# Performance work log

Hardware: AMD Instinct MI355X
Metric: run time of the kernel (lower is better)

The kernel has to match this reference:

```python
import jax, jax.numpy as jnp
import numpy as np


def setup_inputs() -> dict:
    key = jax.random.key(0)
    ks = jax.random.split(key, 8)
    b, l, d, n = 2, 4096, 1024, 16
    s = 0.02
    return {
        "x": jax.random.normal(ks[0], (b, l, d), dtype=jnp.float32),
        "W1": jax.random.normal(ks[1], (d, d), dtype=jnp.float32) * s,
        "b1": jnp.zeros((d,), dtype=jnp.float32),
        "W2": jax.random.normal(ks[2], (n, d), dtype=jnp.float32) * s,
        "b2": jnp.zeros((n,), dtype=jnp.float32),
        "W3": jax.random.normal(ks[3], (n, d), dtype=jnp.float32) * s,
        "b3": jnp.zeros((n,), dtype=jnp.float32),
        "A": jax.random.normal(ks[4], (d, n), dtype=jnp.float32) * s,
    }


def reference(x, W1, b1, W2, b2, W3, b3, A):
    # Faithful to the torch S6.forward as written:
    #   B = fc2(x); C = fc3(x); delta = softplus(fc1(x))
    #   dB = einsum('bld,bln->bldn', delta, B)
    #   h  = dA * 0 + x[..., None] * dB          (h starts at zeros, no scan)
    #   y  = einsum('bln,bldn->bld', C, h)
    # which collapses exactly to y = x * delta * sum_n(C * B).
    # dA = exp(einsum('bld,dn->bldn', delta, A)) is multiplied by zeros and
    # therefore never influences the output (A is a dead parameter here).
    B = jnp.einsum('bld,nd->bln', x, W2) + b2          # (b, l, n)
    C = jnp.einsum('bld,nd->bln', x, W3) + b3          # (b, l, n)
    delta = jax.nn.softplus(jnp.einsum('bld,ed->ble', x, W1) + b1)  # (b, l, d)
    cb = jnp.sum(C * B, axis=-1)                        # (b, l) = sum_n C*B
    y = x * delta * cb[..., None]                       # (b, l, d)
    return y
```

## Files before the change

### kernel.cpp

```cpp
#include <hip/hip_runtime.h>
#include <hip/hip_bf16.h>
#include <stdint.h>

typedef __attribute__((ext_vector_type(8))) short short8;
typedef __attribute__((ext_vector_type(4))) float f32x4;
typedef __attribute__((ext_vector_type(4))) unsigned short us4;

static __device__ __forceinline__ unsigned short f2bf(float f) {
    union { float f; uint32_t u; } v; v.f = f;
    uint32_t u = v.u;
    uint32_t r = u + 0x7FFFu + ((u >> 16) & 1u);
    return (unsigned short)(r >> 16);
}
static __device__ __forceinline__ float bf2f(unsigned short h) {
    union { uint32_t u; float f; } v; v.u = ((uint32_t)h) << 16;
    return v.f;
}

static __device__ __forceinline__ short8 cvt8(float4 a, float4 b) {
    short8 r;
    r[0] = (short)f2bf(a.x); r[1] = (short)f2bf(a.y);
    r[2] = (short)f2bf(a.z); r[3] = (short)f2bf(a.w);
    r[4] = (short)f2bf(b.x); r[5] = (short)f2bf(b.y);
    r[6] = (short)f2bf(b.z); r[7] = (short)f2bf(b.w);
    return r;
}

__global__ __launch_bounds__(256) void convert_w(const float* __restrict__ w1,
                                                 const float* __restrict__ w2,
                                                 const float* __restrict__ w3,
                                                 unsigned short* __restrict__ o1,
                                                 unsigned short* __restrict__ o2,
                                                 unsigned short* __restrict__ o3) {
    int b = blockIdx.x;
    const float* src; unsigned short* dst; int idx;
    if (b < 1024)      { src = w1; dst = o1; idx = b * 256 + threadIdx.x; }
    else if (b < 1040) { src = w2; dst = o2; idx = (b - 1024) * 256 + threadIdx.x; }
    else               { src = w3; dst = o3; idx = (b - 1040) * 256 + threadIdx.x; }
    float4 v = ((const float4*)src)[idx];
    us4 r = { f2bf(v.x), f2bf(v.y), f2bf(v.z), f2bf(v.w) };
    *(us4*)&dst[(size_t)idx * 4] = r;
}

__global__ __launch_bounds__(256) void cb_kernel(
    const float* __restrict__ x,
    const unsigned short* __restrict__ w2b,
    const unsigned short* __restrict__ w3b,
    const float* __restrict__ b2,
    const float* __restrict__ b3,
    unsigned short* __restrict__ xb,
    float* __restrict__ cbo)
{
    __shared__ float red[4][2][16][16];

    const int t = threadIdx.x;
    const int wave = t >> 6, lane = t & 63;
    const int r0 = blockIdx.x * 16;
    const int rrow = lane & 15;
    const int klane = (lane >> 4) * 8;
    const size_t xrow = (size_t)(r0 + rrow) * 1024;
    const int k0 = wave * 256;

    f32x4 accB = {0.f, 0.f, 0.f, 0.f};
    f32x4 accC = {0.f, 0.f, 0.f, 0.f};

#pragma unroll
    for (int ks = 0; ks < 256; ks += 32) {
        const int k = k0 + ks + klane;
        float4 xa = *(const float4*)&x[xrow + k];
        float4 xc = *(const float4*)&x[xrow + k + 4];
        short8 af = cvt8(xa, xc);
        *(short8*)&xb[xrow + k] = af;
        short8 w2f = *(const short8*)&w2b[(size_t)rrow * 1024 + k];
        short8 w3f = *(const short8*)&w3b[(size_t)rrow * 1024 + k];
        accB = __builtin_amdgcn_mfma_f32_16x16x32_bf16(af, w2f, accB, 0, 0, 0);
        accC = __builtin_amdgcn_mfma_f32_16x16x32_bf16(af, w3f, accC, 0, 0, 0);
    }

#pragma unroll
    for (int j = 0; j < 4; ++j) {
        red[wave][0][(lane >> 4) * 4 + j][lane & 15] = accB[j];
        red[wave][1][(lane >> 4) * 4 + j][lane & 15] = accC[j];
    }
    __syncthreads();

    if (wave == 0) {
        const int n = lane & 15;
        const float b2v = b2[n], b3v = b3[n];
        float prod[4];
#pragma unroll
        for (int j = 0; j < 4; ++j) {
            const int row = (lane >> 4) * 4 + j;
            float Bv = red[0][0][row][n] + red[1][0][row][n]
                     + red[2][0][row][n] + red[3][0][row][n] + b2v;
            float Cv = red[0][1][row][n] + red[1][1][row][n]
                     + red[2][1][row][n] + red[3][1][row][n] + b3v;
            prod[j] = Bv * Cv;
        }
#pragma unroll
        for (int off = 1; off < 16; off <<= 1)
#pragma unroll
            for (int j = 0; j < 4; ++j)
                prod[j] += __shfl_xor(prod[j], off, 64);
        if ((lane & 15) == 0) {
#pragma unroll
            for (int j = 0; j < 4; ++j)
                cbo[r0 + (lane >> 4) * 4 + j] = prod[j];
        }
    }
}

__global__ __launch_bounds__(256, 2) void gemm_kernel(
    const unsigned short* __restrict__ xb,
    const unsigned short* __restrict__ w1b,
    const float* __restrict__ b1,
    const float* __restrict__ cb,
    float* __restrict__ y)
{
    __shared__ unsigned short As[2][128 * 64];
    __shared__ unsigned short Bs[2][128 * 64];

    const int wg = blockIdx.x;
    const int nid = (wg & 7) * 64 + (wg >> 3);
    const int row0 = (nid >> 3) * 128;
    const int col0 = (nid & 7) * 128;

    const int t = threadIdx.x;
    const int wid = t >> 6, lane = t & 63;
    const int wm = wid >> 1, wn = wid & 1;

    const int lrow = lane >> 3;
    const int gslot = (lane & 7) ^ lrow;

    f32x4 acc[4][4];
#pragma unroll
    for (int m = 0; m < 4; ++m)
#pragma unroll
        for (int n = 0; n < 4; ++n)
            acc[m][n] = (f32x4){0.f, 0.f, 0.f, 0.f};

    auto STAGE = [&](int b, int kt) {
#pragma unroll
        for (int p = 0; p < 4; ++p) {
            const int grp = p * 4 + wid;
            const int row = grp * 8 + lrow;
            const int gc = kt + gslot * 8;
            const unsigned short* ga = &xb[(size_t)(row0 + row) * 1024 + gc];
            const unsigned short* gb = &w1b[(size_t)(col0 + row) * 1024 + gc];
            __builtin_amdgcn_global_load_lds(
                (const __attribute__((address_space(1))) void*)ga,
                (__attribute__((address_space(3))) void*)&As[b][grp * 512 + lane * 8], 16, 0, 0);
            __builtin_amdgcn_global_load_lds(
                (const __attribute__((address_space(1))) void*)gb,
                (__attribute__((address_space(3))) void*)&Bs[b][grp * 512 + lane * 8], 16, 0, 0);
        }
    };

    STAGE(0, 0);
    asm volatile("s_waitcnt vmcnt(0)" ::: "memory");
    __builtin_amdgcn_s_barrier();
    __builtin_amdgcn_sched_barrier(0);

    const int ro = lane & 15;
    const int sh = lane >> 4;

    for (int tk = 0; tk < 16; ++tk) {
        const int cur = tk & 1;
        if (tk < 15) {
            STAGE(cur ^ 1, (tk + 1) * 64);
            asm volatile("s_waitcnt vmcnt(8)" ::: "memory");
        } else {
            asm volatile("s_waitcnt vmcnt(0)" ::: "memory");
        }
        __builtin_amdgcn_s_barrier();
        __builtin_amdgcn_sched_barrier(0);

        short8 af[2][4], bfr[2][4];
#pragma unroll
        for (int ks = 0; ks < 2; ++ks) {
            const int s = ks * 4 + sh;
#pragma unroll
            for (int m = 0; m < 4; ++m) {
                const int ar = wm * 64 + m * 16 + ro;
                af[ks][m]  = *(const short8*)&As[cur][ar * 64 + ((s ^ (ro & 7)) << 3)];
                const int br = wn * 64 + m * 16 + ro;
                bfr[ks][m] = *(const short8*)&Bs[cur][br * 64 + ((s ^ (ro & 7)) << 3)];
            }
        }
        __builtin_amdgcn_s_setprio(1);
#pragma unroll
        for (int ks = 0; ks < 2; ++ks)
#pragma unroll
            for (int m = 0; m < 4; ++m)
#pragma unroll
                for (int n = 0; n < 4; ++n)
                    acc[m][n] = __builtin_amdgcn_mfma_f32_16x16x32_bf16(af[ks][m], bfr[ks][n], acc[m][n], 0, 0, 0);
        __builtin_amdgcn_s_setprio(0);

        asm volatile("s_waitcnt lgkmcnt(0)" ::: "memory");
        __builtin_amdgcn_s_barrier();
        __builtin_amdgcn_sched_barrier(0);
    }

#pragma unroll
    for (int m = 0; m < 4; ++m) {
        const int grow_base = row0 + wm * 64 + m * 16 + (lane >> 4) * 4;
#pragma unroll
        for (int n = 0; n < 4; ++n) {
            const int gcol = col0 + wn * 64 + n * 16 + (lane & 15);
            const float bv = b1[gcol];
#pragma unroll
            for (int j = 0; j < 4; ++j) {
                const int grow = grow_base + j;
                const float v = acc[m][n][j] + bv;
                const float sp = (v > 15.f) ? v : __logf(1.f + __expf(v));
                const size_t off = (size_t)grow * 1024 + gcol;
                y[off] = bf2f(xb[off]) * sp * cb[grow];
            }
        }
    }
}

extern "C" void kernel_launch(void* const* d_in, const int* in_sizes, int n_in,
                              void* d_out, int out_size, void* d_ws, size_t ws_size,
                              hipStream_t stream) {
    const float* x  = (const float*)d_in[0];
    const float* W1 = (const float*)d_in[1];
    const float* b1 = (const float*)d_in[2];
    const float* W2 = (const float*)d_in[3];
    const float* b2 = (const float*)d_in[4];
    const float* W3 = (const float*)d_in[5];
    const float* b3 = (const float*)d_in[6];

    float* y = (float*)d_out;

    unsigned short* xb  = (unsigned short*)d_ws;
    unsigned short* w1b = xb + (size_t)8192 * 1024;
    unsigned short* w2b = w1b + (size_t)1024 * 1024;
    unsigned short* w3b = w2b + (size_t)16 * 1024;
    float* cbuf = (float*)(w3b + (size_t)16 * 1024);

    convert_w<<<1056, 256, 0, stream>>>(W1, W2, W3, w1b, w2b, w3b);
    cb_kernel<<<512, 256, 0, stream>>>(x, w2b, w3b, b2, b3, xb, cbuf);
    gemm_kernel<<<512, 256, 0, stream>>>(xb, w1b, b1, cbuf, y);
}
```

Baseline: 48.78 us.

## Enlarge GEMM tile to 256x128 with 8 waves and split-phase MFMA

The main GEMM moves from 128x128 tiles with 4 waves to 256x128 tiles with 8 waves (512 threads), halving the grid to 256 blocks. Each wave now computes 128x32, and LDS fragment loads are split into two half-phases with barriers between them. The global-to-LDS staging is rewritten per thread with XOR swizzle, and the initial wait before the loop is removed. The aim is more reuse per loaded tile and better overlap, at the cost of more LDS (96KB), extra barriers per k-step, and only 256 blocks, which may leave CUs underused.

```diff
diff --git a/kernel.cpp b/kernel.cpp
--- a/kernel.cpp
+++ b/kernel.cpp
@@ -110,56 +110,57 @@
     }
 }
 
-__global__ __launch_bounds__(256, 2) void gemm_kernel(
+__global__ __launch_bounds__(512, 2) void gemm_kernel(
     const unsigned short* __restrict__ xb,
     const unsigned short* __restrict__ w1b,
     const float* __restrict__ b1,
     const float* __restrict__ cb,
     float* __restrict__ y)
 {
-    __shared__ unsigned short As[2][128 * 64];
+    __shared__ unsigned short As[2][256 * 64];
     __shared__ unsigned short Bs[2][128 * 64];
 
     const int wg = blockIdx.x;
-    const int nid = (wg & 7) * 64 + (wg >> 3);
-    const int row0 = (nid >> 3) * 128;
+    const int nid = (wg & 7) * 32 + (wg >> 3);
+    const int row0 = (nid >> 3) * 256;
     const int col0 = (nid & 7) * 128;
 
     const int t = threadIdx.x;
     const int wid = t >> 6, lane = t & 63;
-    const int wm = wid >> 1, wn = wid & 1;
-
-    const int lrow = lane >> 3;
-    const int gslot = (lane & 7) ^ lrow;
-
-    f32x4 acc[4][4];
-#pragma unroll
-    for (int m = 0; m < 4; ++m)
-#pragma unroll
-        for (int n = 0; n < 4; ++n)
+    const int wm = wid >> 2, wn = wid & 3;
+
+    const int trow = t >> 3;
+    const int tslot = t & 7;
+
+    f32x4 acc[8][2];
+#pragma unroll
+    for (int m = 0; m < 8; ++m)
+#pragma unroll
+        for (int n = 0; n < 2; ++n)
             acc[m][n] = (f32x4){0.f, 0.f, 0.f, 0.f};
 
     auto STAGE = [&](int b, int kt) {
 #pragma unroll
         for (int p = 0; p < 4; ++p) {
-            const int grp = p * 4 + wid;
-            const int row = grp * 8 + lrow;
-            const int gc = kt + gslot * 8;
-            const unsigned short* ga = &xb[(size_t)(row0 + row) * 1024 + gc];
-            const unsigned short* gb = &w1b[(size_t)(col0 + row) * 1024 + gc];
+            const int r = trow + p * 64;
+            const int gc = kt + ((tslot ^ (r & 7)) << 3);
+            const unsigned short* ga = &xb[(size_t)(row0 + r) * 1024 + gc];
             __builtin_amdgcn_global_load_lds(
                 (const __attribute__((address_space(1))) void*)ga,
-                (__attribute__((address_space(3))) void*)&As[b][grp * 512 + lane * 8], 16, 0, 0);
+                (__attribute__((address_space(3))) void*)&As[b][r * 64 + tslot * 8], 16, 0, 0);
+        }
+#pragma unroll
+        for (int p = 0; p < 2; ++p) {
+            const int r = trow + p * 64;
+            const int gc = kt + ((tslot ^ (r & 7)) << 3);
+            const unsigned short* gb = &w1b[(size_t)(col0 + r) * 1024 + gc];
             __builtin_amdgcn_global_load_lds(
                 (const __attribute__((address_space(1))) void*)gb,
-                (__attribute__((address_space(3))) void*)&Bs[b][grp * 512 + lane * 8], 16, 0, 0);
+                (__attribute__((address_space(3))) void*)&Bs[b][r * 64 + tslot * 8], 16, 0, 0);
         }
     };
 
     STAGE(0, 0);
-    asm volatile("s_waitcnt vmcnt(0)" ::: "memory");
-    __builtin_amdgcn_s_barrier();
-    __builtin_amdgcn_sched_barrier(0);
 
     const int ro = lane & 15;
     const int sh = lane >> 4;
@@ -168,46 +169,66 @@
         const int cur = tk & 1;
         if (tk < 15) {
             STAGE(cur ^ 1, (tk + 1) * 64);
-            asm volatile("s_waitcnt vmcnt(8)" ::: "memory");
+            asm volatile("s_waitcnt vmcnt(6)" ::: "memory");
         } else {
             asm volatile("s_waitcnt vmcnt(0)" ::: "memory");
         }
         __builtin_amdgcn_s_barrier();
         __builtin_amdgcn_sched_barrier(0);
 
-        short8 af[2][4], bfr[2][4];
+        short8 bf[2][2], af[2][4];
 #pragma unroll
         for (int ks = 0; ks < 2; ++ks) {
-            const int s = ks * 4 + sh;
-#pragma unroll
-            for (int m = 0; m < 4; ++m) {
-                const int ar = wm * 64 + m * 16 + ro;
-                af[ks][m]  = *(const short8*)&As[cur][ar * 64 + ((s ^ (ro & 7)) << 3)];
-                const int br = wn * 64 + m * 16 + ro;
-                bfr[ks][m] = *(const short8*)&Bs[cur][br * 64 + ((s ^ (ro & 7)) << 3)];
-            }
-        }
+            const int s = ((ks * 4 + sh) ^ (ro & 7)) << 3;
+#pragma unroll
+            for (int n = 0; n < 2; ++n)
+                bf[ks][n] = *(const short8*)&Bs[cur][(wn * 32 + n * 16 + ro) * 64 + s];
+#pragma unroll
+            for (int m = 0; m < 4; ++m)
+                af[ks][m] = *(const short8*)&As[cur][(wm * 128 + m * 16 + ro) * 64 + s];
+        }
+        asm volatile("s_waitcnt lgkmcnt(0)" ::: "memory");
+        __builtin_amdgcn_sched_barrier(0);
         __builtin_amdgcn_s_setprio(1);
 #pragma unroll
         for (int ks = 0; ks < 2; ++ks)
 #pragma unroll
             for (int m = 0; m < 4; ++m)
 #pragma unroll
-                for (int n = 0; n < 4; ++n)
-                    acc[m][n] = __builtin_amdgcn_mfma_f32_16x16x32_bf16(af[ks][m], bfr[ks][n], acc[m][n], 0, 0, 0);
+                for (int n = 0; n < 2; ++n)
+                    acc[m][n] = __builtin_amdgcn_mfma_f32_16x16x32_bf16(af[ks][m], bf[ks][n], acc[m][n], 0, 0, 0);
         __builtin_amdgcn_s_setprio(0);
-
+        __builtin_amdgcn_s_barrier();
+        __builtin_amdgcn_sched_barrier(0);
+
+#pragma unroll
+        for (int ks = 0; ks < 2; ++ks) {
+            const int s = ((ks * 4 + sh) ^ (ro & 7)) << 3;
+#pragma unroll
+            for (int m = 0; m < 4; ++m)
+                af[ks][m] = *(const short8*)&As[cur][(wm * 128 + (m + 4) * 16 + ro) * 64 + s];
+        }
         asm volatile("s_waitcnt lgkmcnt(0)" ::: "memory");
+        __builtin_amdgcn_sched_barrier(0);
+        __builtin_amdgcn_s_setprio(1);
+#pragma unroll
+        for (int ks = 0; ks < 2; ++ks)
+#pragma unroll
+            for (int m = 0; m < 4; ++m)
+#pragma unroll
+                for (int n = 0; n < 2; ++n)
+                    acc[m + 4][n] = __builtin_amdgcn_mfma_f32_16x16x32_bf16(af[ks][m], bf[ks][n], acc[m + 4][n], 0, 0, 0);
+        __builtin_amdgcn_s_setprio(0);
         __builtin_amdgcn_s_barrier();
         __builtin_amdgcn_sched_barrier(0);
     }
 
 #pragma unroll
-    for (int m = 0; m < 4; ++m) {
-        const int grow_base = row0 + wm * 64 + m * 16 + (lane >> 4) * 4;
-#pragma unroll
-        for (int n = 0; n < 4; ++n) {
-            const int gcol = col0 + wn * 64 + n * 16 + (lane & 15);
+    for (int m = 0; m < 8; ++m) {
+        const int grow_base = row0 + wm * 128 + m * 16 + (lane >> 4) * 4;
+#pragma unroll
+        for (int n = 0; n < 2; ++n) {
+            const int gcol = col0 + wn * 32 + n * 16 + (lane & 15);
             const float bv = b1[gcol];
 #pragma unroll
             for (int j = 0; j < 4; ++j) {
@@ -242,5 +263,5 @@
 
     convert_w<<<1056, 256, 0, stream>>>(W1, W2, W3, w1b, w2b, w3b);
     cb_kernel<<<512, 256, 0, stream>>>(x, w2b, w3b, b2, b3, xb, cbuf);
-    gemm_kernel<<<512, 256, 0, stream>>>(xb, w1b, b1, cbuf, y);
-}
+    gemm_kernel<<<256, 512, 0, stream>>>(xb, w1b, b1, cbuf, y);
+}
```

Measured after the change: 53.31 us. 9.3% more time.
